# Optimization experiments

Measured on AMD Instinct MI355X. Metric: run time of the kernel, lower is better.

Reference implementation:

```python
import jax, jax.numpy as jnp
import numpy as np

PRIMES = (2, 3, 5, 7, 11, 13, 17, 19)
LOGP = tuple(float(np.log(p)) for p in PRIMES)


def setup_inputs() -> dict:
    key = jax.random.key(0)
    x = jax.random.normal(key, (8192, 4096), dtype=jnp.float32)
    return {"x": x}


def reference(x):
    # modulation = sum_p log(p) * roll(x, p, axis=0); out = x + modulation
    mod = jnp.zeros_like(x)
    for p, lp in zip(PRIMES, LOGP):
        mod = mod + jnp.roll(x, shift=p, axis=0) * jnp.asarray(lp, x.dtype)
    return x + mod
```

## Files before the change

kernel.cpp:

```cpp
#include <hip/hip_runtime.h>


#define ROWS 8192
#define COLS 4096
#define COLS4 (COLS / 4)
#define LOG2_COLS4 10
#define R 32
#define MAXSHIFT 19
#define NXCD 8

typedef float f32x4 __attribute__((ext_vector_type(4)));

__constant__ constexpr int   SHIFT[9] = {0, 2, 3, 5, 7, 11, 13, 17, 19};
__constant__ constexpr float COEF[9]  = {
    1.0f,
    0.69314718055994530942f,
    1.09861228866810969140f,
    1.60943791243410037460f,
    1.94591014905531330511f,
    2.39789527279837054406f,
    2.56494935746153673605f,
    2.83321334405621608025f,
    2.94443897916644046001f
};

__global__ __launch_bounds__(256) void spectral_kernel(
    const f32x4* __restrict__ x, f32x4* __restrict__ out) {
  const int sblk = (blockIdx.x & (NXCD - 1)) * (1024 / NXCD) + (blockIdx.x >> 3);
  const int g = sblk * blockDim.x + threadIdx.x;
  const int j = g & (COLS4 - 1);
  const int b = (g >> LOG2_COLS4) * R;

  f32x4 acc[R];
#pragma unroll
  for (int k = 0; k < R; ++k) acc[k] = (f32x4)(0.f);

#pragma unroll
  for (int t = 0; t < R + MAXSHIFT; ++t) {
    const int r = (b - MAXSHIFT + t) & (ROWS - 1);
    const f32x4 v = x[(r << LOG2_COLS4) + j];
#pragma unroll
    for (int s = 0; s < 9; ++s) {
      const int k = t - MAXSHIFT + SHIFT[s];
      if (k >= 0 && k < R) {
        acc[k] = v * COEF[s] + acc[k];
      }
    }
  }

#pragma unroll
  for (int k = 0; k < R; ++k) {
    __builtin_nontemporal_store(acc[k], &out[((b + k) << LOG2_COLS4) + j]);
  }
}

extern "C" void kernel_launch(void* const* d_in, const int* in_sizes, int n_in,
                              void* d_out, int out_size, void* d_ws, size_t ws_size,
                              hipStream_t stream) {
  const f32x4* x = (const f32x4*)d_in[0];
  f32x4* out = (f32x4*)d_out;
  const int total_threads = (ROWS / R) * COLS4;
  const int block = 256;
  const int grid = total_threads / block;
  spectral_kernel<<<grid, block, 0, stream>>>(x, out);
}
```

Measured before the change: 52.34 us.

## Use float2 columns, 16-row tiles, and streaming stores for higher occupancy

```diff
diff --git a/kernel.cpp b/kernel.cpp
--- a/kernel.cpp
+++ b/kernel.cpp
@@ -3,13 +3,13 @@
 
 #define ROWS 8192
 #define COLS 4096
-#define COLS4 (COLS / 4)
-#define LOG2_COLS4 10
-#define R 32
+#define COLS2 (COLS / 2)
+#define LOG2_COLS2 11
+#define R 16
 #define MAXSHIFT 19
 #define NXCD 8
 
-typedef float f32x4 __attribute__((ext_vector_type(4)));
+typedef float f32x2 __attribute__((ext_vector_type(2)));
 
 __constant__ constexpr int   SHIFT[9] = {0, 2, 3, 5, 7, 11, 13, 17, 19};
 __constant__ constexpr float COEF[9]  = {
@@ -24,21 +24,21 @@
     2.94443897916644046001f
 };
 
-__global__ __launch_bounds__(256) void spectral_kernel(
-    const f32x4* __restrict__ x, f32x4* __restrict__ out) {
-  const int sblk = (blockIdx.x & (NXCD - 1)) * (1024 / NXCD) + (blockIdx.x >> 3);
+__global__ __launch_bounds__(256, 8) void spectral_kernel(
+    const f32x2* __restrict__ x, f32x2* __restrict__ out) {
+  const int sblk = (blockIdx.x & (NXCD - 1)) * (4096 / NXCD) + (blockIdx.x >> 3);
   const int g = sblk * blockDim.x + threadIdx.x;
-  const int j = g & (COLS4 - 1);
-  const int b = (g >> LOG2_COLS4) * R;
+  const int j = g & (COLS2 - 1);
+  const int b = (g >> LOG2_COLS2) * R;
 
-  f32x4 acc[R];
+  f32x2 acc[R];
 #pragma unroll
-  for (int k = 0; k < R; ++k) acc[k] = (f32x4)(0.f);
+  for (int k = 0; k < R; ++k) acc[k] = (f32x2)(0.f);
 
 #pragma unroll
   for (int t = 0; t < R + MAXSHIFT; ++t) {
     const int r = (b - MAXSHIFT + t) & (ROWS - 1);
-    const f32x4 v = x[(r << LOG2_COLS4) + j];
+    const f32x2 v = x[(r << LOG2_COLS2) + j];
 #pragma unroll
     for (int s = 0; s < 9; ++s) {
       const int k = t - MAXSHIFT + SHIFT[s];
@@ -46,20 +46,19 @@
         acc[k] = v * COEF[s] + acc[k];
       }
     }
-  }
-
-#pragma unroll
-  for (int k = 0; k < R; ++k) {
-    __builtin_nontemporal_store(acc[k], &out[((b + k) << LOG2_COLS4) + j]);
+    if (t >= MAXSHIFT) {
+      const int k = t - MAXSHIFT;
+      __builtin_nontemporal_store(acc[k], &out[((b + k) << LOG2_COLS2) + j]);
+    }
   }
 }
 
 extern "C" void kernel_launch(void* const* d_in, const int* in_sizes, int n_in,
                               void* d_out, int out_size, void* d_ws, size_t ws_size,
                               hipStream_t stream) {
-  const f32x4* x = (const f32x4*)d_in[0];
-  f32x4* out = (f32x4*)d_out;
-  const int total_threads = (ROWS / R) * COLS4;
+  const f32x2* x = (const f32x2*)d_in[0];
+  f32x2* out = (f32x2*)d_out;
+  const int total_threads = (ROWS / R) * COLS2;
   const int block = 256;
   const int grid = total_threads / block;
   spectral_kernel<<<grid, block, 0, stream>>>(x, out);
```

New measurement: 43.00 us, median of 2. 1.22x faster.
